# Kernel optimization log

Measured on AMD Instinct MI355X. Metric: run time of the kernel, lower is better.

## Reference

```python
import jax, jax.numpy as jnp
import numpy as np

EPS = 1e-5

def _ln(x, g, b):
    mu = jnp.mean(x, axis=-1, keepdims=True)
    var = jnp.var(x, axis=-1, keepdims=True)
    return (x - mu) * jax.lax.rsqrt(var + EPS) * g + b

def setup_inputs() -> dict:
    key = jax.random.key(0)
    ks = jax.random.split(key, 12)
    T, B, D, H = 64, 2048, 512, 512
    seq = jax.random.normal(ks[0], (T, B, D), dtype=jnp.float32)
    ts = jnp.sort(jax.random.uniform(ks[1], (B, T), dtype=jnp.float32) * 10.0, axis=1)
    def xavier(k, shape):
        fan_in, fan_out = shape[1], shape[0]
        lim = float(np.sqrt(6.0 / (fan_in + fan_out)))
        return jax.random.uniform(k, shape, jnp.float32, -lim, lim)
    Wr = xavier(ks[2], (H, D + H)); br = jnp.ones((H,), jnp.float32)   # reset bias init 1.0
    Wz = xavier(ks[3], (H, D + H)); bz = jnp.ones((H,), jnp.float32)   # update bias init 1.0
    Wc = xavier(ks[4], (H, D + H)); bc = jnp.zeros((H,), jnp.float32)
    Wo = xavier(ks[5], (H, H));     bo = jnp.zeros((H,), jnp.float32)  # output projection
    gx = jnp.ones((D,), jnp.float32); bx = jnp.zeros((D,), jnp.float32)  # layer_norm_x
    gh = jnp.ones((H,), jnp.float32); bh = jnp.zeros((H,), jnp.float32)  # layer_norm_h
    gc = jnp.ones((H,), jnp.float32); bcell = jnp.zeros((H,), jnp.float32)  # layer_norm_out (cell)
    gf = jnp.ones((H,), jnp.float32); bf = jnp.zeros((H,), jnp.float32)  # final layer_norm
    return {"seq": seq, "time_stamps": ts,
            "Wr": Wr, "br": br, "Wz": Wz, "bz": bz, "Wc": Wc, "bc": bc,
            "Wo": Wo, "bo": bo, "gx": gx, "bx": bx, "gh": gh, "bh": bh,
            "gc": gc, "bcell": bcell, "gf": gf, "bf": bf}

def _cell(xn, hn, Wr, br, Wz, bz, Wc, bc, gc, bcell):
    # xn: normalized input [B,D]; hn: (normalized, time-scaled) hidden [B,H]
    xh = jnp.concatenate([xn, hn], axis=-1)
    r = jax.nn.sigmoid(xh @ Wr.T + br)
    z = jax.nn.sigmoid(xh @ Wz.T + bz)
    xrh = jnp.concatenate([xn, r * hn], axis=-1)
    h_tilde = jnp.tanh(xrh @ Wc.T + bc)
    h_new = (1.0 - z) * hn + z * h_tilde
    return _ln(h_new, gc, bcell)  # cell output layer norm (dropout is identity in eval)

def reference(seq, time_stamps, Wr, br, Wz, bz, Wc, bc, Wo, bo, gx, bx, gh, bh, gc, bcell, gf, bf):
    T, B, D = seq.shape
    # first step: h is None -> zeros, no LN on h, no time-decay
    x0 = _ln(seq[0], gx, bx)
    h0 = _cell(x0, jnp.zeros((B, Wr.shape[0]), seq.dtype), Wr, br, Wz, bz, Wc, bc, gc, bcell)
    # remaining steps under scan with LN(h) and exp(-dt) decay
    dts = (time_stamps[:, 1:] - time_stamps[:, :-1]).T  # [T-1, B]
    def step(h, inp):
        x_t, dt = inp
        xn = _ln(x_t, gx, bx)
        hn = _ln(h, gh, bh) * jnp.exp(-jnp.clip(dt, 0.0, 10.0))[:, None]
        h_new = _cell(xn, hn, Wr, br, Wz, bz, Wc, bc, gc, bcell)
        return h_new, h_new
    _, rest = jax.lax.scan(step, h0, (seq[1:], dts))
    states = jnp.concatenate([h0[None], rest], axis=0)  # [T,B,H]
    out = jnp.einsum('tbh,oh->tbo', states, Wo) + bo
    out = out + seq  # residual (input_dim == hidden_dim); dropout identity in eval
    return _ln(out, gf, bf)
```

## Files before the change

kernel.cpp:

```cpp
#include <hip/hip_runtime.h>
#include <math.h>

#define TT 64
#define BB 2048

using f32x4   = __attribute__((ext_vector_type(4))) float;
using short8  = __attribute__((ext_vector_type(8))) short;
using short4v = __attribute__((ext_vector_type(4))) short;

__device__ __forceinline__ unsigned short f2bf(float f) {
    unsigned u = __float_as_uint(f);
    u += 0x7FFF + ((u >> 16) & 1);
    return (unsigned short)(u >> 16);
}
__device__ __forceinline__ float bf2f(unsigned short h) {
    return __uint_as_float(((unsigned)h) << 16);
}
__device__ __forceinline__ float sigmoidf_(float v) { return 1.0f / (1.0f + expf(-v)); }
__device__ __forceinline__ float tanhf_(float v)    { return 1.0f - 2.0f / (expf(2.0f * v) + 1.0f); }

__global__ __launch_bounds__(256)
void pack_w2(const float* __restrict__ src, unsigned short* __restrict__ dst,
             int N, int Ksrc, int kbeg, int Kpk) {
    int i = blockIdx.x * 256 + threadIdx.x;
    if (i >= N * Kpk) return;
    int n = i / Kpk, k = i - n * Kpk;
    int dstIdx = ((n >> 4) * (Kpk >> 5) + (k >> 5)) * 512 + (((k >> 3) & 3) * 16 + (n & 15)) * 8 + (k & 7);
    dst[dstIdx] = f2bf(src[(size_t)n * Ksrc + kbeg + k]);
}

__device__ __forceinline__ int pk_idx(int row, int col) {
    int ks = col >> 5, khi = (col >> 3) & 3, j = col & 7;
    return ((ks * 64) + khi * 16 + row) * 8 + j;
}

__device__ __forceinline__ void ln_row_pk(const float* __restrict__ xr,
                                          const float* __restrict__ g,
                                          const float* __restrict__ b,
                                          unsigned short* __restrict__ tile,
                                          int row, int lane) {
    const int c0 = lane * 8;
    float4 v0 = *(const float4*)(xr + c0);
    float4 v1 = *(const float4*)(xr + c0 + 4);
    float s  = v0.x + v0.y + v0.z + v0.w + v1.x + v1.y + v1.z + v1.w;
    float ss = v0.x*v0.x + v0.y*v0.y + v0.z*v0.z + v0.w*v0.w
             + v1.x*v1.x + v1.y*v1.y + v1.z*v1.z + v1.w*v1.w;
#pragma unroll
    for (int m = 32; m > 0; m >>= 1) { s += __shfl_xor(s, m); ss += __shfl_xor(ss, m); }
    const float mean = s * (1.0f / 512.0f);
    const float var  = ss * (1.0f / 512.0f) - mean * mean;
    const float rs   = rsqrtf(var + 1e-5f);
    float4 g0 = *(const float4*)(g + c0);
    float4 g1 = *(const float4*)(g + c0 + 4);
    float4 b0 = *(const float4*)(b + c0);
    float4 b1 = *(const float4*)(b + c0 + 4);
    short8 o;
    o[0] = (short)f2bf((v0.x - mean) * rs * g0.x + b0.x);
    o[1] = (short)f2bf((v0.y - mean) * rs * g0.y + b0.y);
    o[2] = (short)f2bf((v0.z - mean) * rs * g0.z + b0.z);
    o[3] = (short)f2bf((v0.w - mean) * rs * g0.w + b0.w);
    o[4] = (short)f2bf((v1.x - mean) * rs * g1.x + b1.x);
    o[5] = (short)f2bf((v1.y - mean) * rs * g1.y + b1.y);
    o[6] = (short)f2bf((v1.z - mean) * rs * g1.z + b1.z);
    o[7] = (short)f2bf((v1.w - mean) * rs * g1.w + b1.w);
    *(short8*)&tile[(((lane >> 2) * 64) + (lane & 3) * 16 + row) * 8] = o;
}

__global__ __launch_bounds__(512)
void gx_kernel(const float* __restrict__ seq, const float* __restrict__ gxw,
               const float* __restrict__ bxw, const unsigned short* __restrict__ Wx3,
               unsigned short* __restrict__ gx)
{
    __shared__ unsigned short xt[4 * 8192];
    const int tid  = threadIdx.x;
    const int w    = tid >> 6;
    const int lane = tid & 63;
    const size_t m0 = (size_t)blockIdx.x * 64;
    const int t    = (int)(m0 >> 11);
    const int bloc = (int)((m0 & 2047) >> 4);

#pragma unroll
    for (int rr = 0; rr < 8; ++rr) {
        const int r = w * 8 + rr;
        ln_row_pk(seq + (m0 + r) * 512, gxw, bxw, xt + (r >> 4) * 8192, r & 15, lane);
    }
    __syncthreads();

    for (int nt = 0; nt < 3; ++nt) {
        f32x4 acc[4][4] = {};
#pragma unroll 4
        for (int ks = 0; ks < 16; ++ks) {
            short8 a[4], b[4];
#pragma unroll
            for (int mf = 0; mf < 4; ++mf)
                a[mf] = *(const short8*)&xt[mf * 8192 + (ks * 64 + lane) * 8];
#pragma unroll
            for (int nf = 0; nf < 4; ++nf)
                b[nf] = *(const short8*)(Wx3 + (size_t)(nt * 32 + w * 4 + nf) * 8192 + ks * 512 + lane * 8);
#pragma unroll
            for (int mf = 0; mf < 4; ++mf)
#pragma unroll
                for (int nf = 0; nf < 4; ++nf)
                    acc[mf][nf] = __builtin_amdgcn_mfma_f32_16x16x32_bf16(a[mf], b[nf], acc[mf][nf], 0, 0, 0);
        }
#pragma unroll
        for (int mf = 0; mf < 4; ++mf)
#pragma unroll
            for (int nf = 0; nf < 4; ++nf) {
                const size_t base = (((size_t)t * 128 + bloc + mf) * 96 + nt * 32 + w * 4 + nf) * 256 + lane * 4;
                short4v o;
                o[0] = (short)f2bf(acc[mf][nf][0]);
                o[1] = (short)f2bf(acc[mf][nf][1]);
                o[2] = (short)f2bf(acc[mf][nf][2]);
                o[3] = (short)f2bf(acc[mf][nf][3]);
                *(short4v*)&gx[base] = o;
            }
    }
}

template<int SBF, int HOIST>
__global__ __launch_bounds__(512)
void recurrent_kernel(const float* __restrict__ seq, const float* __restrict__ ts,
                      const unsigned short* __restrict__ Wrz, const unsigned short* __restrict__ Wc,
                      const float* __restrict__ br, const float* __restrict__ bz,
                      const float* __restrict__ bc,
                      const float* __restrict__ gxw, const float* __restrict__ bxw,
                      const float* __restrict__ gh, const float* __restrict__ bh,
                      const float* __restrict__ gc, const float* __restrict__ bcl,
                      const unsigned short* __restrict__ gx,
                      float* __restrict__ states_f32, unsigned short* __restrict__ states_pk)
{
    __shared__ unsigned short hn_s[16 * 512];
    __shared__ unsigned short rh_s[16 * 512];
    __shared__ unsigned short xn_s[HOIST ? 64 : 16 * 512];
    __shared__ float red_s[16][9];
    __shared__ float red_q[16][9];

    const int tid  = threadIdx.x;
    const int w    = tid >> 6;
    const int lane = tid & 63;
    const int lhi  = lane >> 4;
    const int llo  = lane & 15;
    const int m0   = blockIdx.x * 16;

    for (int i = tid; i < 1024; i += 512) *(short8*)&hn_s[i * 8] = short8{};
    if (!HOIST) {
#pragma unroll
        for (int rr = 0; rr < 2; ++rr) {
            const int r = w * 2 + rr;
            ln_row_pk(seq + (size_t)(m0 + r) * 512, gxw, bxw, xn_s, r, lane);
        }
    }
    __syncthreads();

    for (int t = 0; t < TT; ++t) {
        const unsigned short* gxt = HOIST ? gx + (((size_t)t * 128 + blockIdx.x) * 96) * 256 + lane * 4 : nullptr;

        {
            f32x4 aR[4], aZ[4];
            if (HOIST) {
#pragma unroll
                for (int f = 0; f < 4; ++f) {
                    short4v g1 = *(const short4v*)(gxt + (size_t)(w * 4 + f) * 256);
                    short4v g2 = *(const short4v*)(gxt + (size_t)(32 + w * 4 + f) * 256);
#pragma unroll
                    for (int i = 0; i < 4; ++i) {
                        aR[f][i] = bf2f((unsigned short)g1[i]);
                        aZ[f][i] = bf2f((unsigned short)g2[i]);
                    }
                }
#pragma unroll 4
                for (int ks = 0; ks < 16; ++ks) {
                    short8 a = *(const short8*)&hn_s[(ks * 64 + lane) * 8];
                    const int off = ks * 512 + lane * 8;
#pragma unroll
                    for (int f = 0; f < 4; ++f) {
                        short8 b1 = *(const short8*)(Wrz + (size_t)(w * 4 + f) * 8192 + off);
                        aR[f] = __builtin_amdgcn_mfma_f32_16x16x32_bf16(a, b1, aR[f], 0, 0, 0);
                        short8 b2 = *(const short8*)(Wrz + (size_t)(32 + w * 4 + f) * 8192 + off);
                        aZ[f] = __builtin_amdgcn_mfma_f32_16x16x32_bf16(a, b2, aZ[f], 0, 0, 0);
                    }
                }
            } else {
#pragma unroll
                for (int f = 0; f < 4; ++f) { aR[f] = f32x4{}; aZ[f] = f32x4{}; }
#pragma unroll 2
                for (int ks = 0; ks < 32; ++ks) {
                    short8 a = (ks < 16) ? *(const short8*)&xn_s[(ks * 64 + lane) * 8]
                                         : *(const short8*)&hn_s[((ks - 16) * 64 + lane) * 8];
                    const int off = ks * 512 + lane * 8;
#pragma unroll
                    for (int f = 0; f < 4; ++f) {
                        short8 b1 = *(const short8*)(Wrz + (size_t)(w * 4 + f) * 16384 + off);
                        aR[f] = __builtin_amdgcn_mfma_f32_16x16x32_bf16(a, b1, aR[f], 0, 0, 0);
                        short8 b2 = *(const short8*)(Wrz + (size_t)(32 + w * 4 + f) * 16384 + off);
                        aZ[f] = __builtin_amdgcn_mfma_f32_16x16x32_bf16(a, b2, aZ[f], 0, 0, 0);
                    }
                }
            }
#pragma unroll
            for (int f = 0; f < 4; ++f)
#pragma unroll
                for (int i = 0; i < 4; ++i) {
                    const int row = lhi * 4 + i;
                    const int col = w * 64 + f * 16 + llo;
                    const float rr = sigmoidf_(aR[f][i] + br[col]);
                    const float hv = bf2f(hn_s[pk_idx(row, col)]);
                    rh_s[pk_idx(row, col)] = f2bf(rr * hv);
                    aR[f][i] = sigmoidf_(aZ[f][i] + bz[col]);
                }
            __syncthreads();

            f32x4 aC[4];
            if (HOIST) {
#pragma unroll
                for (int f = 0; f < 4; ++f) {
                    short4v g3 = *(const short4v*)(gxt + (size_t)(64 + w * 4 + f) * 256);
#pragma unroll
                    for (int i = 0; i < 4; ++i) aC[f][i] = bf2f((unsigned short)g3[i]);
                }
#pragma unroll 4
                for (int ks = 0; ks < 16; ++ks) {
                    short8 a = *(const short8*)&rh_s[(ks * 64 + lane) * 8];
                    const int off = ks * 512 + lane * 8;
#pragma unroll
                    for (int f = 0; f < 4; ++f) {
                        short8 b1 = *(const short8*)(Wc + (size_t)(w * 4 + f) * 8192 + off);
                        aC[f] = __builtin_amdgcn_mfma_f32_16x16x32_bf16(a, b1, aC[f], 0, 0, 0);
                    }
                }
            } else {
#pragma unroll
                for (int f = 0; f < 4; ++f) aC[f] = f32x4{};
#pragma unroll 2
                for (int ks = 0; ks < 32; ++ks) {
                    short8 a = (ks < 16) ? *(const short8*)&xn_s[(ks * 64 + lane) * 8]
                                         : *(const short8*)&rh_s[((ks - 16) * 64 + lane) * 8];
                    const int off = ks * 512 + lane * 8;
#pragma unroll
                    for (int f = 0; f < 4; ++f) {
                        short8 b1 = *(const short8*)(Wc + (size_t)(w * 4 + f) * 16384 + off);
                        aC[f] = __builtin_amdgcn_mfma_f32_16x16x32_bf16(a, b1, aC[f], 0, 0, 0);
                    }
                }
            }
            __syncthreads();

            float hnew[4][4];
#pragma unroll
            for (int f = 0; f < 4; ++f)
#pragma unroll
                for (int i = 0; i < 4; ++i) {
                    const int row = lhi * 4 + i;
                    const int col = w * 64 + f * 16 + llo;
                    const float htil = tanhf_(aC[f][i] + bc[col]);
                    const float hv = bf2f(hn_s[pk_idx(row, col)]);
                    const float z = aR[f][i];
                    hnew[f][i] = (1.0f - z) * hv + z * htil;
                }
#pragma unroll
            for (int i = 0; i < 4; ++i) {
                float s = hnew[0][i] + hnew[1][i] + hnew[2][i] + hnew[3][i];
                float q = hnew[0][i]*hnew[0][i] + hnew[1][i]*hnew[1][i]
                        + hnew[2][i]*hnew[2][i] + hnew[3][i]*hnew[3][i];
#pragma unroll
                for (int m = 8; m >= 1; m >>= 1) { s += __shfl_xor(s, m); q += __shfl_xor(q, m); }
                if (llo == 0) { red_s[lhi * 4 + i][w] = s; red_q[lhi * 4 + i][w] = q; }
            }
            __syncthreads();
            float mu[4], rsd[4];
#pragma unroll
            for (int i = 0; i < 4; ++i) {
                float s = 0.f, q = 0.f;
#pragma unroll
                for (int w2 = 0; w2 < 8; ++w2) { s += red_s[lhi * 4 + i][w2]; q += red_q[lhi * 4 + i][w2]; }
                const float m_ = s * (1.0f / 512.0f);
                mu[i]  = m_;
                rsd[i] = rsqrtf(q * (1.0f / 512.0f) - m_ * m_ + 1e-5f);
            }
#pragma unroll
            for (int f = 0; f < 4; ++f)
#pragma unroll
                for (int i = 0; i < 4; ++i) {
                    const int row = lhi * 4 + i;
                    const int col = w * 64 + f * 16 + llo;
                    const float h = (hnew[f][i] - mu[i]) * rsd[i] * gc[col] + bcl[col];
                    if (SBF) states_pk[((size_t)t * 128 + blockIdx.x) * 8192 + pk_idx(row, col)] = f2bf(h);
                    else     states_f32[(size_t)t * BB * 512 + (size_t)(m0 + row) * 512 + col] = h;
                    hnew[f][i] = h;
                }
            if (t + 1 < TT) {
                __syncthreads();
#pragma unroll
                for (int i = 0; i < 4; ++i) {
                    float s = hnew[0][i] + hnew[1][i] + hnew[2][i] + hnew[3][i];
                    float q = hnew[0][i]*hnew[0][i] + hnew[1][i]*hnew[1][i]
                            + hnew[2][i]*hnew[2][i] + hnew[3][i]*hnew[3][i];
#pragma unroll
                    for (int m = 8; m >= 1; m >>= 1) { s += __shfl_xor(s, m); q += __shfl_xor(q, m); }
                    if (llo == 0) { red_s[lhi * 4 + i][w] = s; red_q[lhi * 4 + i][w] = q; }
                }
                __syncthreads();
                float dec_[4];
#pragma unroll
                for (int i = 0; i < 4; ++i) {
                    float s = 0.f, q = 0.f;
#pragma unroll
                    for (int w2 = 0; w2 < 8; ++w2) { s += red_s[lhi * 4 + i][w2]; q += red_q[lhi * 4 + i][w2]; }
                    const float m_ = s * (1.0f / 512.0f);
                    mu[i]  = m_;
                    rsd[i] = rsqrtf(q * (1.0f / 512.0f) - m_ * m_ + 1e-5f);
                    const int grow = m0 + lhi * 4 + i;
                    float dtv = ts[(size_t)grow * TT + t + 1] - ts[(size_t)grow * TT + t];
                    dtv = fminf(fmaxf(dtv, 0.0f), 10.0f);
                    dec_[i] = expf(-dtv);
                }
#pragma unroll
                for (int f = 0; f < 4; ++f)
#pragma unroll
                    for (int i = 0; i < 4; ++i) {
                        const int row = lhi * 4 + i;
                        const int col = w * 64 + f * 16 + llo;
                        const float hv = ((hnew[f][i] - mu[i]) * rsd[i] * gh[col] + bh[col]) * dec_[i];
                        hn_s[pk_idx(row, col)] = f2bf(hv);
                    }
                if (!HOIST) {
#pragma unroll
                    for (int rr = 0; rr < 2; ++rr) {
                        const int r = w * 2 + rr;
                        ln_row_pk(seq + ((size_t)(t + 1) * BB + m0 + r) * 512, gxw, bxw, xn_s, r, lane);
                    }
                }
            }
        }
        __syncthreads();
    }
}

template<int BF>
__global__ __launch_bounds__(512)
void proj_kernel(const float* __restrict__ S, const unsigned short* __restrict__ Spk,
                 const unsigned short* __restrict__ Wo, const float* __restrict__ bo,
                 const float* __restrict__ seq, const float* __restrict__ gf,
                 const float* __restrict__ bff, float* __restrict__ out)
{
    const int tid  = threadIdx.x;
    const int wave = tid >> 6;
    const int lane = tid & 63;
    const int lhi  = lane >> 4;
    const int llo  = lane & 15;
    const long m0  = (long)blockIdx.x * 64;
    const int t    = (int)(m0 >> 11);
    const int blk  = (int)((m0 & 2047) >> 4);

    f32x4 acc[4][4] = {};
#pragma unroll 2
    for (int ks = 0; ks < 16; ++ks) {
        short8 a[4], b[4];
#pragma unroll
        for (int mf = 0; mf < 4; ++mf) {
            if (BF) {
                a[mf] = *(const short8*)(Spk + ((size_t)t * 128 + blk + mf) * 8192 + (ks * 64 + lane) * 8);
            } else {
                const float* ap = S + (size_t)(m0 + mf * 16 + llo) * 512 + ks * 32 + lhi * 8;
                float4 f0 = *(const float4*)ap;
                float4 f1 = *(const float4*)(ap + 4);
                short8 av;
                av[0] = (short)f2bf(f0.x); av[1] = (short)f2bf(f0.y);
                av[2] = (short)f2bf(f0.z); av[3] = (short)f2bf(f0.w);
                av[4] = (short)f2bf(f1.x); av[5] = (short)f2bf(f1.y);
                av[6] = (short)f2bf(f1.z); av[7] = (short)f2bf(f1.w);
                a[mf] = av;
            }
        }
#pragma unroll
        for (int nf = 0; nf < 4; ++nf)
            b[nf] = *(const short8*)(Wo + (size_t)(wave * 4 + nf) * 8192 + ks * 512 + lane * 8);
#pragma unroll
        for (int mf = 0; mf < 4; ++mf)
#pragma unroll
            for (int nf = 0; nf < 4; ++nf)
                acc[mf][nf] = __builtin_amdgcn_mfma_f32_16x16x32_bf16(a[mf], b[nf], acc[mf][nf], 0, 0, 0);
    }

    __shared__ float red_s[64][9];
    __shared__ float red_q[64][9];

#pragma unroll
    for (int mf = 0; mf < 4; ++mf)
#pragma unroll
        for (int i = 0; i < 4; ++i) {
            const long row = m0 + mf * 16 + lhi * 4 + i;
#pragma unroll
            for (int nf = 0; nf < 4; ++nf) {
                const int col = wave * 64 + nf * 16 + llo;
                acc[mf][nf][i] += bo[col] + seq[(size_t)row * 512 + col];
            }
        }
    float mu[4][4], rstd[4][4];
#pragma unroll
    for (int mf = 0; mf < 4; ++mf)
#pragma unroll
        for (int i = 0; i < 4; ++i) {
            float s = 0.f, q = 0.f;
#pragma unroll
            for (int nf = 0; nf < 4; ++nf) { const float v = acc[mf][nf][i]; s += v; q += v * v; }
#pragma unroll
            for (int m = 8; m >= 1; m >>= 1) { s += __shfl_xor(s, m); q += __shfl_xor(q, m); }
            if (llo == 0) { red_s[mf * 16 + lhi * 4 + i][wave] = s; red_q[mf * 16 + lhi * 4 + i][wave] = q; }
        }
    __syncthreads();
#pragma unroll
    for (int mf = 0; mf < 4; ++mf)
#pragma unroll
        for (int i = 0; i < 4; ++i) {
            const int rl = mf * 16 + lhi * 4 + i;
            float s = 0.f, q = 0.f;
#pragma unroll
            for (int w2 = 0; w2 < 8; ++w2) { s += red_s[rl][w2]; q += red_q[rl][w2]; }
            const float m_ = s * (1.0f / 512.0f);
            mu[mf][i] = m_;
            rstd[mf][i] = rsqrtf(q * (1.0f / 512.0f) - m_ * m_ + 1e-5f);
        }
#pragma unroll
    for (int mf = 0; mf < 4; ++mf)
#pragma unroll
        for (int i = 0; i < 4; ++i) {
            const long row = m0 + mf * 16 + lhi * 4 + i;
#pragma unroll
            for (int nf = 0; nf < 4; ++nf) {
                const int col = wave * 64 + nf * 16 + llo;
                out[(size_t)row * 512 + col] = (acc[mf][nf][i] - mu[mf][i]) * rstd[mf][i] * gf[col] + bff[col];
            }
        }
}

extern "C" void kernel_launch(void* const* d_in, const int* in_sizes, int n_in,
                              void* d_out, int out_size, void* d_ws, size_t ws_size,
                              hipStream_t stream) {
    const float* seq = (const float*)d_in[0];
    const float* ts  = (const float*)d_in[1];
    const float* Wr  = (const float*)d_in[2];
    const float* br  = (const float*)d_in[3];
    const float* Wz  = (const float*)d_in[4];
    const float* bz  = (const float*)d_in[5];
    const float* Wc  = (const float*)d_in[6];
    const float* bc  = (const float*)d_in[7];
    const float* Wo  = (const float*)d_in[8];
    const float* bo  = (const float*)d_in[9];
    const float* gx  = (const float*)d_in[10];
    const float* bx  = (const float*)d_in[11];
    const float* gh  = (const float*)d_in[12];
    const float* bh  = (const float*)d_in[13];
    const float* gc  = (const float*)d_in[14];
    const float* bcl = (const float*)d_in[15];
    const float* gf  = (const float*)d_in[16];
    const float* bf  = (const float*)d_in[17];
    float* out = (float*)d_out;

    char* w0 = (char*)d_ws;
    char* w = w0;
    unsigned short* Wrz_full = (unsigned short*)w; w += (size_t)1024 * 1024 * 2;
    unsigned short* Wc_full  = (unsigned short*)w; w += (size_t)512 * 1024 * 2;
    unsigned short* Wrz_h    = (unsigned short*)w; w += (size_t)1024 * 512 * 2;
    unsigned short* Wc_h     = (unsigned short*)w; w += (size_t)512 * 512 * 2;
    unsigned short* Wx3      = (unsigned short*)w; w += (size_t)1536 * 512 * 2;
    unsigned short* Wo_pk    = (unsigned short*)w; w += (size_t)512 * 512 * 2;

    const size_t GXB = (size_t)TT * 128 * 96 * 256 * 2;
    const size_t SBB = (size_t)TT * 128 * 8192 * 2;

    const bool hoist = ws_size >= (size_t)(w - w0) + GXB;
    unsigned short* gxbuf = (unsigned short*)w;
    if (hoist) w += GXB;
    const bool sbf = ws_size >= (size_t)(w - w0) + SBB;
    unsigned short* states_pk = (unsigned short*)w;

    if (hoist) {
        pack_w2<<<1024, 256, 0, stream>>>(Wr, Wrz_h, 512, 1024, 512, 512);
        pack_w2<<<1024, 256, 0, stream>>>(Wz, Wrz_h + (size_t)512 * 512, 512, 1024, 512, 512);
        pack_w2<<<1024, 256, 0, stream>>>(Wc, Wc_h, 512, 1024, 512, 512);
        pack_w2<<<1024, 256, 0, stream>>>(Wr, Wx3, 512, 1024, 0, 512);
        pack_w2<<<1024, 256, 0, stream>>>(Wz, Wx3 + (size_t)512 * 512, 512, 1024, 0, 512);
        pack_w2<<<1024, 256, 0, stream>>>(Wc, Wx3 + (size_t)2 * 512 * 512, 512, 1024, 0, 512);
    } else {
        pack_w2<<<2048, 256, 0, stream>>>(Wr, Wrz_full, 512, 1024, 0, 1024);
        pack_w2<<<2048, 256, 0, stream>>>(Wz, Wrz_full + (size_t)512 * 1024, 512, 1024, 0, 1024);
        pack_w2<<<2048, 256, 0, stream>>>(Wc, Wc_full, 512, 1024, 0, 1024);
    }
    pack_w2<<<1024, 256, 0, stream>>>(Wo, Wo_pk, 512, 512, 0, 512);

    if (hoist)
        gx_kernel<<<2048, 512, 0, stream>>>(seq, gx, bx, Wx3, gxbuf);

    const unsigned short* Wa = hoist ? Wrz_h : Wrz_full;
    const unsigned short* Wb = hoist ? Wc_h  : Wc_full;
    if (hoist) {
        if (sbf) recurrent_kernel<1,1><<<128, 512, 0, stream>>>(seq, ts, Wa, Wb, br, bz, bc, gx, bx, gh, bh, gc, bcl, gxbuf, out, states_pk);
        else     recurrent_kernel<0,1><<<128, 512, 0, stream>>>(seq, ts, Wa, Wb, br, bz, bc, gx, bx, gh, bh, gc, bcl, gxbuf, out, states_pk);
    } else {
        if (sbf) recurrent_kernel<1,0><<<128, 512, 0, stream>>>(seq, ts, Wa, Wb, br, bz, bc, gx, bx, gh, bh, gc, bcl, gxbuf, out, states_pk);
        else     recurrent_kernel<0,0><<<128, 512, 0, stream>>>(seq, ts, Wa, Wb, br, bz, bc, gx, bx, gh, bh, gc, bcl, gxbuf, out, states_pk);
    }

    if (sbf)
        proj_kernel<1><<<2048, 512, 0, stream>>>(nullptr, states_pk, Wo_pk, bo, seq, gf, bf, out);
    else
        proj_kernel<0><<<2048, 512, 0, stream>>>(out, nullptr, Wo_pk, bo, seq, gf, bf, out);
}
```

Before: 1.792 ms.

## Fuse weight packing launches and add padded row-major hidden copy in LDS

```diff
diff --git a/kernel.cpp b/kernel.cpp
--- a/kernel.cpp
+++ b/kernel.cpp
@@ -27,6 +27,29 @@
     int n = i / Kpk, k = i - n * Kpk;
     int dstIdx = ((n >> 4) * (Kpk >> 5) + (k >> 5)) * 512 + (((k >> 3) & 3) * 16 + (n & 15)) * 8 + (k & 7);
     dst[dstIdx] = f2bf(src[(size_t)n * Ksrc + kbeg + k]);
+}
+
+__global__ __launch_bounds__(256)
+void pack_all(const float* __restrict__ Wr, const float* __restrict__ Wz,
+              const float* __restrict__ Wc, const float* __restrict__ Wo,
+              unsigned short* __restrict__ Wrz_h, unsigned short* __restrict__ Wc_h,
+              unsigned short* __restrict__ Wx3, unsigned short* __restrict__ Wo_pk) {
+    int i = blockIdx.x * 256 + threadIdx.x;
+    int seg = i >> 18;
+    int r = i & 262143;
+    int n = r >> 9, k = r & 511;
+    int dstIdx = ((n >> 4) * 16 + (k >> 5)) * 512 + (((k >> 3) & 3) * 16 + (n & 15)) * 8 + (k & 7);
+    const float* src; unsigned short* dst; int kb, Ksrc;
+    switch (seg) {
+        case 0: src = Wr; dst = Wrz_h;               kb = 512; Ksrc = 1024; break;
+        case 1: src = Wz; dst = Wrz_h + 262144;      kb = 512; Ksrc = 1024; break;
+        case 2: src = Wc; dst = Wc_h;                kb = 512; Ksrc = 1024; break;
+        case 3: src = Wr; dst = Wx3;                 kb = 0;   Ksrc = 1024; break;
+        case 4: src = Wz; dst = Wx3 + 262144;        kb = 0;   Ksrc = 1024; break;
+        case 5: src = Wc; dst = Wx3 + 2 * 262144;    kb = 0;   Ksrc = 1024; break;
+        default: src = Wo; dst = Wo_pk;              kb = 0;   Ksrc = 512;  break;
+    }
+    dst[dstIdx] = f2bf(src[(size_t)n * Ksrc + kb + k]);
 }
 
 __device__ __forceinline__ int pk_idx(int row, int col) {
@@ -132,6 +155,7 @@
 {
     __shared__ unsigned short hn_s[16 * 512];
     __shared__ unsigned short rh_s[16 * 512];
+    __shared__ unsigned short hn2_s[16 * 520];
     __shared__ unsigned short xn_s[HOIST ? 64 : 16 * 512];
     __shared__ float red_s[16][9];
     __shared__ float red_q[16][9];
@@ -144,6 +168,7 @@
     const int m0   = blockIdx.x * 16;
 
     for (int i = tid; i < 1024; i += 512) *(short8*)&hn_s[i * 8] = short8{};
+    for (int i = tid; i < 16 * 520; i += 512) hn2_s[i] = 0;
     if (!HOIST) {
 #pragma unroll
         for (int rr = 0; rr < 2; ++rr) {
@@ -205,7 +230,7 @@
                     const int row = lhi * 4 + i;
                     const int col = w * 64 + f * 16 + llo;
                     const float rr = sigmoidf_(aR[f][i] + br[col]);
-                    const float hv = bf2f(hn_s[pk_idx(row, col)]);
+                    const float hv = bf2f(hn2_s[row * 520 + col]);
                     rh_s[pk_idx(row, col)] = f2bf(rr * hv);
                     aR[f][i] = sigmoidf_(aZ[f][i] + bz[col]);
                 }
@@ -254,7 +279,7 @@
                     const int row = lhi * 4 + i;
                     const int col = w * 64 + f * 16 + llo;
                     const float htil = tanhf_(aC[f][i] + bc[col]);
-                    const float hv = bf2f(hn_s[pk_idx(row, col)]);
+                    const float hv = bf2f(hn2_s[row * 520 + col]);
                     const float z = aR[f][i];
                     hnew[f][i] = (1.0f - z) * hv + z * htil;
                 }
@@ -323,6 +348,7 @@
                         const int col = w * 64 + f * 16 + llo;
                         const float hv = ((hnew[f][i] - mu[i]) * rsd[i] * gh[col] + bh[col]) * dec_[i];
                         hn_s[pk_idx(row, col)] = f2bf(hv);
+                        hn2_s[row * 520 + col] = f2bf(hv);
                     }
                 if (!HOIST) {
 #pragma unroll
@@ -477,18 +503,13 @@
     unsigned short* states_pk = (unsigned short*)w;
 
     if (hoist) {
-        pack_w2<<<1024, 256, 0, stream>>>(Wr, Wrz_h, 512, 1024, 512, 512);
-        pack_w2<<<1024, 256, 0, stream>>>(Wz, Wrz_h + (size_t)512 * 512, 512, 1024, 512, 512);
-        pack_w2<<<1024, 256, 0, stream>>>(Wc, Wc_h, 512, 1024, 512, 512);
-        pack_w2<<<1024, 256, 0, stream>>>(Wr, Wx3, 512, 1024, 0, 512);
-        pack_w2<<<1024, 256, 0, stream>>>(Wz, Wx3 + (size_t)512 * 512, 512, 1024, 0, 512);
-        pack_w2<<<1024, 256, 0, stream>>>(Wc, Wx3 + (size_t)2 * 512 * 512, 512, 1024, 0, 512);
+        pack_all<<<7168, 256, 0, stream>>>(Wr, Wz, Wc, Wo, Wrz_h, Wc_h, Wx3, Wo_pk);
     } else {
         pack_w2<<<2048, 256, 0, stream>>>(Wr, Wrz_full, 512, 1024, 0, 1024);
         pack_w2<<<2048, 256, 0, stream>>>(Wz, Wrz_full + (size_t)512 * 1024, 512, 1024, 0, 1024);
         pack_w2<<<2048, 256, 0, stream>>>(Wc, Wc_full, 512, 1024, 0, 1024);
-    }
-    pack_w2<<<1024, 256, 0, stream>>>(Wo, Wo_pk, 512, 512, 0, 512);
+        pack_w2<<<1024, 256, 0, stream>>>(Wo, Wo_pk, 512, 512, 0, 512);
+    }
 
     if (hoist)
         gx_kernel<<<2048, 512, 0, stream>>>(seq, gx, bx, Wx3, gxbuf);
```

Measured after the change: 2.397 ms. 33.8% more time.
